# Performance work log

Measured on AMD Instinct MI355X. Metric: run time of the kernel, lower is better.

Reference implementation:

```python
import jax, jax.numpy as jnp
import numpy as np

B, S, E, H, U = 2048, 64, 512, 512, 512

def setup_inputs() -> dict:
    key = jax.random.key(0)
    ks = jax.random.split(key, 6)
    s = lambda d: 1.0 / np.sqrt(d)
    return {
        "features": jax.random.normal(ks[0], (B, S, E), jnp.float32),
        "hidden": jax.random.normal(ks[1], (B, H), jnp.float32),
        "W1": jax.random.normal(ks[2], (E, U), jnp.float32) * s(E),
        "b1": jnp.zeros((U,), jnp.float32),
        "W2": jax.random.normal(ks[3], (H, U), jnp.float32) * s(H),
        "b2": jnp.zeros((U,), jnp.float32),
        "Wv": jax.random.normal(ks[4], (U, 1), jnp.float32) * s(U),
        "bv": jnp.zeros((1,), jnp.float32),
    }

def reference(features, hidden, W1, b1, W2, b2, Wv, bv):
    # Bahdanau additive attention (dropout at inference = identity).
    h1 = jnp.einsum('bse,eu->bsu', features, W1) + b1          # [B,S,U]
    h2 = hidden @ W2 + b2                                       # [B,U]
    scores = jnp.tanh(h1 + h2[:, None, :]) @ Wv + bv            # [B,S,1]
    weights = jax.nn.softmax(scores, axis=1)                    # softmax over seq
    context = jnp.sum(weights * features, axis=1)               # [B,E]
    return context
```

## Files before the change

### kernel.cpp

```cpp
#include <hip/hip_runtime.h>

typedef _Float16 f16x8 __attribute__((ext_vector_type(8)));
typedef float f32x4 __attribute__((ext_vector_type(4)));

#define KDIM 512
#define UDIM 512

#define VMWAIT(N) asm volatile("s_waitcnt vmcnt(" #N ")" ::: "memory")
#define LGKM0()   asm volatile("s_waitcnt lgkmcnt(0)" ::: "memory")
#define FENCE()   asm volatile("" ::: "memory")
#define BAR()     do { __builtin_amdgcn_s_barrier(); FENCE(); } while (0)

__device__ __forceinline__ void cvt_store_a(unsigned short* dst, float4 a0, float4 a1) {
    f16x8 h8;
    h8[0] = (_Float16)a0.x; h8[1] = (_Float16)a0.y;
    h8[2] = (_Float16)a0.z; h8[3] = (_Float16)a0.w;
    h8[4] = (_Float16)a1.x; h8[5] = (_Float16)a1.y;
    h8[6] = (_Float16)a1.z; h8[7] = (_Float16)a1.w;
    *(f16x8*)dst = h8;
}

__global__ void convert_w_kernel(const float* __restrict__ w1,
                                 const float* __restrict__ w2,
                                 unsigned short* __restrict__ w1img,
                                 unsigned short* __restrict__ w2img) {
    int u = blockIdx.x;
    int k = threadIdx.x + blockIdx.y * 256;
    size_t idx = (size_t)(k >> 5) * 16384 + (size_t)u * 32 + (k & 31);
    _Float16 h1 = (_Float16)w1[(size_t)k * UDIM + u];
    _Float16 h2 = (_Float16)w2[(size_t)k * UDIM + u];
    w1img[idx] = __builtin_bit_cast(unsigned short, h1);
    w2img[idx] = __builtin_bit_cast(unsigned short, h2);
}

__device__ __forceinline__ void gemm_pipe_64x512(
    const float* __restrict__ aSrc, const char* __restrict__ bImg,
    unsigned short* As, f32x4 acc[4][8])
{
    const int tid = threadIdx.x;
    const int lane = tid & 63, wid = tid >> 6;
    const int lane16 = lane & 15, g = lane >> 4;

    const int s_row = tid >> 2, s_ks = tid & 3;
    const float* aptr = aSrc + (size_t)s_row * KDIM + s_ks * 8;
    const int a_widx = s_row * 32 + ((s_ks ^ ((s_row >> 1) & 3)) << 3);

    int aoff[4];
    #pragma unroll
    for (int i = 0; i < 4; ++i) {
        int r = i * 16 + lane16;
        aoff[i] = r * 32 + ((g ^ ((r >> 1) & 3)) << 3);
    }
    const char* bbase = bImg + (size_t)(wid * 128 + lane16) * 64 + g * 16;

    #pragma unroll
    for (int i = 0; i < 4; ++i)
        #pragma unroll
        for (int j = 0; j < 8; ++j) acc[i][j] = (f32x4){0.f, 0.f, 0.f, 0.f};

    f16x8 brA[8], brB[8];
    #pragma unroll
    for (int j = 0; j < 8; ++j) brA[j] = *(const f16x8*)(bbase + j * 1024);
    FENCE();
    #pragma unroll
    for (int j = 0; j < 8; ++j) brB[j] = *(const f16x8*)(bbase + 32768 + j * 1024);
    FENCE();
    float4 aE0 = *(const float4*)(aptr);
    float4 aE1 = *(const float4*)(aptr + 4);
    FENCE();
    float4 aO0 = *(const float4*)(aptr + 32);
    float4 aO1 = *(const float4*)(aptr + 36);
    FENCE();
    VMWAIT(2);
    cvt_store_a(As + a_widx, aE0, aE1);
    aE0 = *(const float4*)(aptr + 64);
    aE1 = *(const float4*)(aptr + 68);
    FENCE();
    LGKM0(); BAR();

#define PSTEP(T, CUR, BR, AC0, AC1, DO_CVT, DO_A, DO_B, DO_BAR) do {            \
    if (DO_CVT) cvt_store_a(As + ((CUR) ^ 1) * 2048 + a_widx, AC0, AC1);         \
    if (DO_A) { AC0 = *(const float4*)(aptr + ((T) + 3) * 32);                   \
                AC1 = *(const float4*)(aptr + ((T) + 3) * 32 + 4); }             \
    FENCE();                                                                     \
    __builtin_amdgcn_s_setprio(1);                                               \
    _Pragma("unroll")                                                            \
    for (int i_ = 0; i_ < 4; ++i_) {                                             \
        f16x8 af_ = *(const f16x8*)(As + (CUR) * 2048 + aoff[i_]);               \
        _Pragma("unroll")                                                        \
        for (int j_ = 0; j_ < 8; ++j_)                                           \
            acc[i_][j_] = __builtin_amdgcn_mfma_f32_16x16x32_f16(                \
                af_, BR[j_], acc[i_][j_], 0, 0, 0);                              \
    }                                                                            \
    __builtin_amdgcn_s_setprio(0);                                               \
    if (DO_B) { _Pragma("unroll")                                                \
        for (int j_ = 0; j_ < 8; ++j_)                                           \
            BR[j_] = *(const f16x8*)(bbase + ((T) + 2) * 32768 + j_ * 1024); }   \
    if (DO_BAR) { LGKM0(); BAR(); }                                              \
} while (0)

    VMWAIT(2);  PSTEP(0, 0, brA, aO0, aO1, true, true, true, true);
    #pragma unroll 1
    for (int i = 0; i < 6; ++i) {
        const int t = 2 * i + 1;
        VMWAIT(10); PSTEP(t,     1, brB, aE0, aE1, true, true, true, true);
        VMWAIT(10); PSTEP(t + 1, 0, brA, aO0, aO1, true, true, true, true);
    }
    VMWAIT(10); PSTEP(13, 1, brB, aE0, aE1, true,  false, true,  true);
    VMWAIT(8);  PSTEP(14, 0, brA, aO0, aO1, true,  false, false, true);
    VMWAIT(0);  PSTEP(15, 1, brB, aE0, aE1, false, false, false, false);
#undef PSTEP
}

__global__ __launch_bounds__(256, 2)
void h2_gemm_f16_kernel(const float* __restrict__ hidden,
                        const char* __restrict__ w2img,
                        const float* __restrict__ b2,
                        float* __restrict__ h2) {
    __shared__ unsigned short As[2 * 2048];
    const int tid = threadIdx.x, bm = blockIdx.x;
    const int lane = tid & 63, wid = tid >> 6;
    const int lane16 = lane & 15, g = lane >> 4;

    f32x4 acc[4][8];
    gemm_pipe_64x512(hidden + (size_t)bm * 64 * KDIM, w2img, As, acc);

    #pragma unroll
    for (int j = 0; j < 8; ++j) {
        int col = wid * 128 + j * 16 + lane16;
        float bb = b2[col];
        #pragma unroll
        for (int i = 0; i < 4; ++i)
            #pragma unroll
            for (int r = 0; r < 4; ++r) {
                int row = bm * 64 + i * 16 + g * 4 + r;
                h2[(size_t)row * UDIM + col] = acc[i][j][r] + bb;
            }
    }
}

__global__ __launch_bounds__(256, 2)
void fused_all_kernel(const float* __restrict__ feat,
                      const char* __restrict__ w1img,
                      const float* __restrict__ h2,
                      const float* __restrict__ b1,
                      const float* __restrict__ wv,
                      float* __restrict__ out) {
    __shared__ unsigned short As[2 * 2048];
    __shared__ float spl[64 * 4];
    __shared__ float wsm[64];

    const int tid = threadIdx.x;
    const int bm = blockIdx.x;
    const int lane = tid & 63, wid = tid >> 6;
    const int lane16 = lane & 15, g = lane >> 4;

    f32x4 acc[4][8];
    gemm_pipe_64x512(feat + (size_t)bm * 64 * KDIM, w1img, As, acc);

    float hhv[8], wvv[8];
    #pragma unroll
    for (int j = 0; j < 8; ++j) {
        int u = wid * 128 + j * 16 + lane16;
        hhv[j] = b1[u] + h2[(size_t)bm * UDIM + u];
        wvv[j] = wv[u];
    }

    #pragma unroll
    for (int i = 0; i < 4; ++i) {
        #pragma unroll
        for (int r = 0; r < 4; ++r) {
            float s = 0.f;
            #pragma unroll
            for (int j = 0; j < 8; ++j) {
                float h = acc[i][j][r] + hhv[j];
                float ex = __expf(2.f * h);
                float th = 1.f - 2.f * __builtin_amdgcn_rcpf(ex + 1.f);
                s += th * wvv[j];
            }
            s += __shfl_xor(s, 1); s += __shfl_xor(s, 2);
            s += __shfl_xor(s, 4); s += __shfl_xor(s, 8);
            if (lane16 == 0)
                spl[(i * 16 + g * 4 + r) * 4 + wid] = s;
        }
    }
    __syncthreads();

    if (tid < 64) {
        float s = (spl[tid * 4 + 0] + spl[tid * 4 + 1]) +
                  (spl[tid * 4 + 2] + spl[tid * 4 + 3]);
        float m = s;
        #pragma unroll
        for (int off = 32; off; off >>= 1) m = fmaxf(m, __shfl_xor(m, off));
        float e = __expf(s - m);
        float sum = e;
        #pragma unroll
        for (int off = 32; off; off >>= 1) sum += __shfl_xor(sum, off);
        wsm[tid] = e / sum;
    }
    __syncthreads();

    {
        const float2* f2 = (const float2*)(feat + (size_t)bm * 64 * KDIM);
        float ax = 0.f, ay = 0.f;
        #pragma unroll 8
        for (int s = 0; s < 64; ++s) {
            float w = wsm[s];
            float2 v = f2[s * 256 + tid];
            ax += w * v.x; ay += w * v.y;
        }
        ((float2*)out)[(size_t)bm * 256 + tid] = make_float2(ax, ay);
    }
}

extern "C" void kernel_launch(void* const* d_in, const int* in_sizes, int n_in,
                              void* d_out, int out_size, void* d_ws, size_t ws_size,
                              hipStream_t stream) {
    (void)in_sizes; (void)n_in; (void)out_size; (void)ws_size;
    const float* feat   = (const float*)d_in[0];
    const float* hidden = (const float*)d_in[1];
    const float* W1     = (const float*)d_in[2];
    const float* b1     = (const float*)d_in[3];
    const float* W2     = (const float*)d_in[4];
    const float* b2     = (const float*)d_in[5];
    const float* Wv     = (const float*)d_in[6];
    float* out = (float*)d_out;

    char* ws = (char*)d_ws;
    unsigned short* w1img = (unsigned short*)(ws);
    unsigned short* w2img = (unsigned short*)(ws + 524288);
    float* h2 = (float*)(ws + 1048576);

    convert_w_kernel<<<dim3(512, 2), dim3(256), 0, stream>>>(W1, W2, w1img, w2img);
    h2_gemm_f16_kernel<<<dim3(32), dim3(256), 0, stream>>>(hidden, (const char*)w2img, b2, h2);
    fused_all_kernel<<<dim3(2048), dim3(256), 0, stream>>>(feat, (const char*)w1img, h2, b1, Wv, out);
}
```

Before: 155.1 us.

## Stage whole fp16 feature tile in LDS and reuse it for context sum

Each block now converts its full 64x512 feature tile to fp16 into 64KB of LDS up front, instead of streaming K-slices through a double buffer. The GEMM is then done in two 64-column chunks with register double-buffering of A and B fragments and no barriers inside the K loop. The final weighted sum reads the fp16 features from LDS rather than re-reading fp32 features from global memory. This removes the second global read of the features and the per-step barriers, at the cost of lower occupancy from the 64KB LDS and fp16 precision in the context sum.

```diff
diff --git a/kernel.cpp b/kernel.cpp
--- a/kernel.cpp
+++ b/kernel.cpp
@@ -1,24 +1,10 @@
 #include <hip/hip_runtime.h>
 
 typedef _Float16 f16x8 __attribute__((ext_vector_type(8)));
+typedef unsigned short u16x4 __attribute__((ext_vector_type(4)));
 typedef float f32x4 __attribute__((ext_vector_type(4)));
 
-#define KDIM 512
-#define UDIM 512
-
 #define VMWAIT(N) asm volatile("s_waitcnt vmcnt(" #N ")" ::: "memory")
-#define LGKM0()   asm volatile("s_waitcnt lgkmcnt(0)" ::: "memory")
-#define FENCE()   asm volatile("" ::: "memory")
-#define BAR()     do { __builtin_amdgcn_s_barrier(); FENCE(); } while (0)
-
-__device__ __forceinline__ void cvt_store_a(unsigned short* dst, float4 a0, float4 a1) {
-    f16x8 h8;
-    h8[0] = (_Float16)a0.x; h8[1] = (_Float16)a0.y;
-    h8[2] = (_Float16)a0.z; h8[3] = (_Float16)a0.w;
-    h8[4] = (_Float16)a1.x; h8[5] = (_Float16)a1.y;
-    h8[6] = (_Float16)a1.z; h8[7] = (_Float16)a1.w;
-    *(f16x8*)dst = h8;
-}
 
 __global__ void convert_w_kernel(const float* __restrict__ w1,
                                  const float* __restrict__ w2,
@@ -27,115 +13,127 @@
     int u = blockIdx.x;
     int k = threadIdx.x + blockIdx.y * 256;
     size_t idx = (size_t)(k >> 5) * 16384 + (size_t)u * 32 + (k & 31);
-    _Float16 h1 = (_Float16)w1[(size_t)k * UDIM + u];
-    _Float16 h2 = (_Float16)w2[(size_t)k * UDIM + u];
+    _Float16 h1 = (_Float16)w1[(size_t)k * 512 + u];
+    _Float16 h2 = (_Float16)w2[(size_t)k * 512 + u];
     w1img[idx] = __builtin_bit_cast(unsigned short, h1);
     w2img[idx] = __builtin_bit_cast(unsigned short, h2);
 }
 
-__device__ __forceinline__ void gemm_pipe_64x512(
-    const float* __restrict__ aSrc, const char* __restrict__ bImg,
-    unsigned short* As, f32x4 acc[4][8])
-{
-    const int tid = threadIdx.x;
-    const int lane = tid & 63, wid = tid >> 6;
-    const int lane16 = lane & 15, g = lane >> 4;
-
-    const int s_row = tid >> 2, s_ks = tid & 3;
-    const float* aptr = aSrc + (size_t)s_row * KDIM + s_ks * 8;
-    const int a_widx = s_row * 32 + ((s_ks ^ ((s_row >> 1) & 3)) << 3);
-
-    int aoff[4];
-    #pragma unroll
-    for (int i = 0; i < 4; ++i) {
-        int r = i * 16 + lane16;
-        aoff[i] = r * 32 + ((g ^ ((r >> 1) & 3)) << 3);
-    }
-    const char* bbase = bImg + (size_t)(wid * 128 + lane16) * 64 + g * 16;
-
-    #pragma unroll
-    for (int i = 0; i < 4; ++i)
-        #pragma unroll
-        for (int j = 0; j < 8; ++j) acc[i][j] = (f32x4){0.f, 0.f, 0.f, 0.f};
-
-    f16x8 brA[8], brB[8];
-    #pragma unroll
-    for (int j = 0; j < 8; ++j) brA[j] = *(const f16x8*)(bbase + j * 1024);
-    FENCE();
-    #pragma unroll
-    for (int j = 0; j < 8; ++j) brB[j] = *(const f16x8*)(bbase + 32768 + j * 1024);
-    FENCE();
-    float4 aE0 = *(const float4*)(aptr);
-    float4 aE1 = *(const float4*)(aptr + 4);
-    FENCE();
-    float4 aO0 = *(const float4*)(aptr + 32);
-    float4 aO1 = *(const float4*)(aptr + 36);
-    FENCE();
-    VMWAIT(2);
-    cvt_store_a(As + a_widx, aE0, aE1);
-    aE0 = *(const float4*)(aptr + 64);
-    aE1 = *(const float4*)(aptr + 68);
-    FENCE();
-    LGKM0(); BAR();
-
-#define PSTEP(T, CUR, BR, AC0, AC1, DO_CVT, DO_A, DO_B, DO_BAR) do {            \
-    if (DO_CVT) cvt_store_a(As + ((CUR) ^ 1) * 2048 + a_widx, AC0, AC1);         \
-    if (DO_A) { AC0 = *(const float4*)(aptr + ((T) + 3) * 32);                   \
-                AC1 = *(const float4*)(aptr + ((T) + 3) * 32 + 4); }             \
-    FENCE();                                                                     \
-    __builtin_amdgcn_s_setprio(1);                                               \
-    _Pragma("unroll")                                                            \
-    for (int i_ = 0; i_ < 4; ++i_) {                                             \
-        f16x8 af_ = *(const f16x8*)(As + (CUR) * 2048 + aoff[i_]);               \
-        _Pragma("unroll")                                                        \
-        for (int j_ = 0; j_ < 8; ++j_)                                           \
-            acc[i_][j_] = __builtin_amdgcn_mfma_f32_16x16x32_f16(                \
-                af_, BR[j_], acc[i_][j_], 0, 0, 0);                              \
-    }                                                                            \
-    __builtin_amdgcn_s_setprio(0);                                               \
-    if (DO_B) { _Pragma("unroll")                                                \
-        for (int j_ = 0; j_ < 8; ++j_)                                           \
-            BR[j_] = *(const f16x8*)(bbase + ((T) + 2) * 32768 + j_ * 1024); }   \
-    if (DO_BAR) { LGKM0(); BAR(); }                                              \
-} while (0)
-
-    VMWAIT(2);  PSTEP(0, 0, brA, aO0, aO1, true, true, true, true);
-    #pragma unroll 1
-    for (int i = 0; i < 6; ++i) {
-        const int t = 2 * i + 1;
-        VMWAIT(10); PSTEP(t,     1, brB, aE0, aE1, true, true, true, true);
-        VMWAIT(10); PSTEP(t + 1, 0, brA, aO0, aO1, true, true, true, true);
-    }
-    VMWAIT(10); PSTEP(13, 1, brB, aE0, aE1, true,  false, true,  true);
-    VMWAIT(8);  PSTEP(14, 0, brA, aO0, aO1, true,  false, false, true);
-    VMWAIT(0);  PSTEP(15, 1, brB, aE0, aE1, false, false, false, false);
-#undef PSTEP
+__device__ __forceinline__ void stage_a64(const float* __restrict__ src,
+                                          char* As, int tid) {
+    const int row = tid >> 2, q = tid & 3;
+    const float* p = src + (size_t)row * 512 + q * 4;
+    const int sw2 = ((row >> 1) & 3) << 4;
+    char* wb = As + row * 64;
+    float4 va[4], vb[4];
+#define AISS(V, G) { _Pragma("unroll") \
+    for (int j_ = 0; j_ < 4; ++j_) V[j_] = *(const float4*)(p + ((G) * 4 + j_) * 16); }
+#define APRC(V, G) { _Pragma("unroll") \
+    for (int j_ = 0; j_ < 4; ++j_) { \
+        const int i_ = (G) * 4 + j_; \
+        u16x4 h_; \
+        h_[0] = __builtin_bit_cast(unsigned short, (_Float16)V[j_].x); \
+        h_[1] = __builtin_bit_cast(unsigned short, (_Float16)V[j_].y); \
+        h_[2] = __builtin_bit_cast(unsigned short, (_Float16)V[j_].z); \
+        h_[3] = __builtin_bit_cast(unsigned short, (_Float16)V[j_].w); \
+        *(u16x4*)(wb + (i_ >> 1) * 4096 + ((q * 8 + (i_ & 1) * 32) ^ sw2)) = h_; } }
+    AISS(va, 0); AISS(vb, 1);
+    VMWAIT(4); APRC(va, 0); AISS(va, 2);
+    VMWAIT(4); APRC(vb, 1); AISS(vb, 3);
+    VMWAIT(4); APRC(va, 2); AISS(va, 4);
+    VMWAIT(4); APRC(vb, 3); AISS(vb, 5);
+    VMWAIT(4); APRC(va, 4); AISS(va, 6);
+    VMWAIT(4); APRC(vb, 5); AISS(vb, 7);
+    VMWAIT(4); APRC(va, 6);
+    VMWAIT(0); APRC(vb, 7);
+#undef AISS
+#undef APRC
+}
+
+__device__ __forceinline__ void chunk_gemm(const char* __restrict__ bcol,
+                                           const char* As, const int* aoff,
+                                           f32x4 acc[4][4]) {
+    f16x8 brA[4], brB[4], afA[4], afB[4];
+    #pragma unroll
+    for (int i = 0; i < 4; ++i)
+        #pragma unroll
+        for (int j = 0; j < 4; ++j) acc[i][j] = (f32x4){0.f, 0.f, 0.f, 0.f};
+    #pragma unroll
+    for (int j = 0; j < 4; ++j) brA[j] = *(const f16x8*)(bcol + j * 1024);
+    #pragma unroll
+    for (int j = 0; j < 4; ++j) brB[j] = *(const f16x8*)(bcol + 32768 + j * 1024);
+    #pragma unroll
+    for (int i = 0; i < 4; ++i) afA[i] = *(const f16x8*)(As + aoff[i]);
+
+    #pragma unroll
+    for (int tt = 0; tt < 8; ++tt) {
+        const int t0 = 2 * tt, t1 = t0 + 1;
+        if (t0 < 15) {
+            #pragma unroll
+            for (int i = 0; i < 4; ++i)
+                afB[i] = *(const f16x8*)(As + t1 * 4096 + aoff[i]);
+        }
+        VMWAIT(4);
+        #pragma unroll
+        for (int i = 0; i < 4; ++i)
+            #pragma unroll
+            for (int j = 0; j < 4; ++j)
+                acc[i][j] = __builtin_amdgcn_mfma_f32_16x16x32_f16(afA[i], brA[j], acc[i][j], 0, 0, 0);
+        if (t0 < 14) {
+            #pragma unroll
+            for (int j = 0; j < 4; ++j)
+                brA[j] = *(const f16x8*)(bcol + (t0 + 2) * 32768 + j * 1024);
+        }
+        if (t1 < 15) {
+            #pragma unroll
+            for (int i = 0; i < 4; ++i)
+                afA[i] = *(const f16x8*)(As + (t1 + 1) * 4096 + aoff[i]);
+        }
+        if (t1 < 14) { VMWAIT(4); } else { VMWAIT(0); }
+        #pragma unroll
+        for (int i = 0; i < 4; ++i)
+            #pragma unroll
+            for (int j = 0; j < 4; ++j)
+                acc[i][j] = __builtin_amdgcn_mfma_f32_16x16x32_f16(afB[i], brB[j], acc[i][j], 0, 0, 0);
+        if (t1 < 14) {
+            #pragma unroll
+            for (int j = 0; j < 4; ++j)
+                brB[j] = *(const f16x8*)(bcol + (t1 + 2) * 32768 + j * 1024);
+        }
+    }
 }
 
 __global__ __launch_bounds__(256, 2)
-void h2_gemm_f16_kernel(const float* __restrict__ hidden,
-                        const char* __restrict__ w2img,
-                        const float* __restrict__ b2,
-                        float* __restrict__ h2) {
-    __shared__ unsigned short As[2 * 2048];
+void h2_gemm_kernel(const float* __restrict__ hidden,
+                    const char* __restrict__ w2img,
+                    const float* __restrict__ b2,
+                    float* __restrict__ h2o) {
+    __shared__ char As[65536];
     const int tid = threadIdx.x, bm = blockIdx.x;
     const int lane = tid & 63, wid = tid >> 6;
     const int lane16 = lane & 15, g = lane >> 4;
-
-    f32x4 acc[4][8];
-    gemm_pipe_64x512(hidden + (size_t)bm * 64 * KDIM, w2img, As, acc);
-
-    #pragma unroll
-    for (int j = 0; j < 8; ++j) {
-        int col = wid * 128 + j * 16 + lane16;
-        float bb = b2[col];
-        #pragma unroll
-        for (int i = 0; i < 4; ++i)
-            #pragma unroll
-            for (int r = 0; r < 4; ++r) {
-                int row = bm * 64 + i * 16 + g * 4 + r;
-                h2[(size_t)row * UDIM + col] = acc[i][j][r] + bb;
-            }
+    stage_a64(hidden + (size_t)bm * 32768, As, tid);
+    __syncthreads();
+    const int swA = (lane16 >> 1) & 3;
+    int aoff[4];
+    #pragma unroll
+    for (int i = 0; i < 4; ++i)
+        aoff[i] = (i * 16 + lane16) * 64 + ((g ^ swA) << 4);
+    #pragma unroll
+    for (int c = 0; c < 2; ++c) {
+        const char* bcol = w2img + (size_t)(wid * 128 + c * 64 + lane16) * 64 + g * 16;
+        f32x4 acc[4][4];
+        chunk_gemm(bcol, As, aoff, acc);
+        #pragma unroll
+        for (int j = 0; j < 4; ++j) {
+            int col = wid * 128 + c * 64 + j * 16 + lane16;
+            float bb = b2[col];
+            #pragma unroll
+            for (int i = 0; i < 4; ++i)
+                #pragma unroll
+                for (int r = 0; r < 4; ++r)
+                    h2o[(size_t)(bm * 64 + i * 16 + g * 4 + r) * 512 + col] = acc[i][j][r] + bb;
+        }
     }
 }
 
@@ -146,44 +144,64 @@
                       const float* __restrict__ b1,
                       const float* __restrict__ wv,
                       float* __restrict__ out) {
-    __shared__ unsigned short As[2 * 2048];
-    __shared__ float spl[64 * 4];
+    __shared__ char As[65536];
+    __shared__ float spl[256];
     __shared__ float wsm[64];
-
-    const int tid = threadIdx.x;
-    const int bm = blockIdx.x;
+    const int tid = threadIdx.x, bm = blockIdx.x;
     const int lane = tid & 63, wid = tid >> 6;
     const int lane16 = lane & 15, g = lane >> 4;
 
-    f32x4 acc[4][8];
-    gemm_pipe_64x512(feat + (size_t)bm * 64 * KDIM, w1img, As, acc);
+    stage_a64(feat + (size_t)bm * 32768, As, tid);
+    __syncthreads();
 
     float hhv[8], wvv[8];
     #pragma unroll
     for (int j = 0; j < 8; ++j) {
         int u = wid * 128 + j * 16 + lane16;
-        hhv[j] = b1[u] + h2[(size_t)bm * UDIM + u];
+        hhv[j] = b1[u] + h2[(size_t)bm * 512 + u];
         wvv[j] = wv[u];
     }
-
-    #pragma unroll
-    for (int i = 0; i < 4; ++i) {
+    VMWAIT(0);
+
+    const int swA = (lane16 >> 1) & 3;
+    int aoff[4];
+    #pragma unroll
+    for (int i = 0; i < 4; ++i)
+        aoff[i] = (i * 16 + lane16) * 64 + ((g ^ swA) << 4);
+
+    float sacc[16];
+    #pragma unroll
+    for (int x = 0; x < 16; ++x) sacc[x] = 0.f;
+
+    #pragma unroll
+    for (int c = 0; c < 2; ++c) {
+        const char* bcol = w1img + (size_t)(wid * 128 + c * 64 + lane16) * 64 + g * 16;
+        f32x4 acc[4][4];
+        chunk_gemm(bcol, As, aoff, acc);
+        #pragma unroll
+        for (int i = 0; i < 4; ++i)
+            #pragma unroll
+            for (int r = 0; r < 4; ++r) {
+                float s = 0.f;
+                #pragma unroll
+                for (int j = 0; j < 4; ++j) {
+                    float h = acc[i][j][r] + hhv[c * 4 + j];
+                    float ex = __expf(2.f * h);
+                    s += (1.f - 2.f * __builtin_amdgcn_rcpf(ex + 1.f)) * wvv[c * 4 + j];
+                }
+                sacc[i * 4 + r] += s;
+            }
+    }
+
+    #pragma unroll
+    for (int i = 0; i < 4; ++i)
         #pragma unroll
         for (int r = 0; r < 4; ++r) {
-            float s = 0.f;
-            #pragma unroll
-            for (int j = 0; j < 8; ++j) {
-                float h = acc[i][j][r] + hhv[j];
-                float ex = __expf(2.f * h);
-                float th = 1.f - 2.f * __builtin_amdgcn_rcpf(ex + 1.f);
-                s += th * wvv[j];
-            }
+            float s = sacc[i * 4 + r];
             s += __shfl_xor(s, 1); s += __shfl_xor(s, 2);
             s += __shfl_xor(s, 4); s += __shfl_xor(s, 8);
-            if (lane16 == 0)
-                spl[(i * 16 + g * 4 + r) * 4 + wid] = s;
-        }
-    }
+            if (lane16 == 0) spl[(i * 16 + g * 4 + r) * 4 + wid] = s;
+        }
     __syncthreads();
 
     if (tid < 64) {
@@ -201,13 +219,16 @@
     __syncthreads();
 
     {
-        const float2* f2 = (const float2*)(feat + (size_t)bm * 64 * KDIM);
+        const int cseg = (tid >> 4) * 4096;
+        const int cin = (tid & 15) * 4;
         float ax = 0.f, ay = 0.f;
         #pragma unroll 8
         for (int s = 0; s < 64; ++s) {
+            unsigned v = *(const unsigned*)(As + cseg + s * 64 +
+                                            (cin ^ (((s >> 1) & 3) << 4)));
             float w = wsm[s];
-            float2 v = f2[s * 256 + tid];
-            ax += w * v.x; ay += w * v.y;
+            ax += w * (float)__builtin_bit_cast(_Float16, (unsigned short)(v & 0xffffu));
+            ay += w * (float)__builtin_bit_cast(_Float16, (unsigned short)(v >> 16));
         }
         ((float2*)out)[(size_t)bm * 256 + tid] = make_float2(ax, ay);
     }
@@ -232,6 +253,6 @@
     float* h2 = (float*)(ws + 1048576);
 
     convert_w_kernel<<<dim3(512, 2), dim3(256), 0, stream>>>(W1, W2, w1img, w2img);
-    h2_gemm_f16_kernel<<<dim3(32), dim3(256), 0, stream>>>(hidden, (const char*)w2img, b2, h2);
+    h2_gemm_kernel<<<dim3(32), dim3(256), 0, stream>>>(hidden, (const char*)w2img, b2, h2);
     fused_all_kernel<<<dim3(2048), dim3(256), 0, stream>>>(feat, (const char*)w1img, h2, b1, Wv, out);
 }
```

Measured after the change: 149.6 us. -3.6%, faster.
